# Performance work log

Measured on AMD Instinct MI355X. Metric: run time of the kernel, lower is better.

The kernel has to match this reference:

```python
import jax, jax.numpy as jnp
import numpy as np

LOG2 = float(np.log(2.0))

def ssp(v):
    # shifted softplus: log(0.5*e^v + 0.5)
    return jax.nn.softplus(v) - jnp.asarray(LOG2, v.dtype)

def lora_dense(h, W, b, A, B):
    # base GEMM + per-sample (modulated) low-rank correction; scale = alpha/rank = 1
    base = jnp.einsum('b...i,io->b...o', h, W) + b
    lora = jnp.einsum('b...r,bro->b...o', jnp.einsum('b...i,bir->b...r', h, A), B)
    return ssp(base + lora)

def setup_inputs() -> dict:
    key = jax.random.key(0)
    ks = jax.random.split(key, 32)
    Bsz, Atoms, F, Rbf, R = 2, 512, 128, 64, 4
    d = {}
    d['x'] = jax.random.normal(ks[0], (Bsz, Atoms, F), jnp.float32)
    d['f_ij'] = jax.random.uniform(ks[1], (Bsz, Atoms, Atoms, Rbf), jnp.float32)
    d['c_ij'] = jax.random.uniform(ks[2], (Bsz, Atoms, Atoms), jnp.float32)
    d['mask'] = jax.random.randint(ks[3], (Bsz, Atoms, Atoms), 0, 2, jnp.int32)
    def mk(i, din, dout):
        return (jax.random.normal(ks[4+4*i], (din, dout), jnp.float32) * (1.0/np.sqrt(din)),
                jnp.zeros((dout,), jnp.float32),
                jax.random.normal(ks[5+4*i], (Bsz, din, R), jnp.float32) * 0.05,
                jax.random.normal(ks[6+4*i], (Bsz, R, dout), jnp.float32) * 0.05)
    d['W_bc'], d['b_bc'], d['A_bc'], d['B_bc'] = mk(0, F, F)      # atomwise_bc: F -> dim_filter(=F)
    d['W_f0'], d['b_f0'], d['A_f0'], d['B_f0'] = mk(1, Rbf, F)    # dis_filter layer0
    d['W_f1'], d['b_f1'], d['A_f1'], d['B_f1'] = mk(2, F, F)      # dis_filter layer1
    d['W_f2'], d['b_f2'], d['A_f2'], d['B_f2'] = mk(3, F, F)      # dis_filter layer2
    d['W_a0'], d['b_a0'], d['A_a0'], d['B_a0'] = mk(4, F, F)      # atomwise_ac layer0
    d['W_a1'], d['b_a1'], d['A_a1'], d['B_a1'] = mk(5, F, F)      # atomwise_ac layer1
    return d

def reference(x, f_ij, c_ij, mask,
              W_bc, b_bc, A_bc, B_bc,
              W_f0, b_f0, A_f0, B_f0,
              W_f1, b_f1, A_f1, B_f1,
              W_f2, b_f2, A_f2, B_f2,
              W_a0, b_a0, A_a0, B_a0,
              W_a1, b_a1, A_a1, B_a1):
    x_i = lora_dense(x, W_bc, b_bc, A_bc, B_bc)                 # (B, A, Fdim)
    h = lora_dense(f_ij, W_f0, b_f0, A_f0, B_f0)                # (B, A, A, Fdim)
    h = lora_dense(h, W_f1, b_f1, A_f1, B_f1)
    h = lora_dense(h, W_f2, b_f2, A_f2, B_f2)
    w_ij = h * c_ij[..., None]                                  # (B, A, A, Fdim)
    # x_ij = expand_dims(x_i, -3): neighbor-j features broadcast over receiver i
    y = x_i[:, None, :, :] * w_ij                               # (B, A, A, Fdim)
    y = y * mask[..., None].astype(y.dtype)
    y = jnp.sum(y, axis=-2)                                     # masked neighbor sum -> (B, A, Fdim)
    y = lora_dense(y, W_a0, b_a0, A_a0, B_a0)
    y = lora_dense(y, W_a1, b_a1, A_a1, B_a1)
    return x + y
```

## Files before the change

### kernel.cpp

```cpp
#include <hip/hip_runtime.h>
#include <hip/hip_bf16.h>


typedef float        f32x4  __attribute__((ext_vector_type(4)));
typedef unsigned int u32x4  __attribute__((ext_vector_type(4)));
typedef unsigned int u32x2  __attribute__((ext_vector_type(2)));
typedef __bf16       bf16x8 __attribute__((ext_vector_type(8)));

__device__ __forceinline__ float ssp_pre(float acc, float bpre) {
  float t = __builtin_amdgcn_exp2f(__builtin_fmaf(acc, 1.44269504089f, bpre));
  return 0.69314718056f * __builtin_amdgcn_logf(__builtin_fmaf(t, 0.5f, 0.5f));
}

__device__ __forceinline__ float ssp_f(float v) {
  float t = __builtin_amdgcn_exp2f(v * 1.44269504089f);
  return 0.69314718056f * __builtin_amdgcn_logf(__builtin_fmaf(t, 0.5f, 0.5f));
}

__device__ __forceinline__ unsigned short f2bfu(float f) {
  __hip_bfloat16 h = __float2bfloat16(f);
  return __builtin_bit_cast(unsigned short, h);
}

__device__ __forceinline__ u32x4 pack8(f32x4 a, f32x4 b) {
  u32x4 u;
  u.x = (unsigned)f2bfu(a.x) | ((unsigned)f2bfu(a.y) << 16);
  u.y = (unsigned)f2bfu(a.z) | ((unsigned)f2bfu(a.w) << 16);
  u.z = (unsigned)f2bfu(b.x) | ((unsigned)f2bfu(b.y) << 16);
  u.w = (unsigned)f2bfu(b.z) | ((unsigned)f2bfu(b.w) << 16);
  return u;
}

__device__ __forceinline__ f32x4 fzero4() { f32x4 z = {0.f, 0.f, 0.f, 0.f}; return z; }

#define SWZ(j) (((j) & 7) << 4)

__global__ void prep_weights(
    const float* __restrict__ W_bc, const float* __restrict__ A_bc, const float* __restrict__ B_bc,
    const float* __restrict__ W_f0, const float* __restrict__ A_f0, const float* __restrict__ B_f0,
    const float* __restrict__ W_f1, const float* __restrict__ A_f1, const float* __restrict__ B_f1,
    const float* __restrict__ W_f2, const float* __restrict__ A_f2, const float* __restrict__ B_f2,
    const float* __restrict__ W_a0, const float* __restrict__ A_a0, const float* __restrict__ B_a0,
    const float* __restrict__ W_a1, const float* __restrict__ A_a1, const float* __restrict__ B_a1,
    unsigned short* __restrict__ Wt0, unsigned short* __restrict__ Wt1, unsigned short* __restrict__ Wt2,
    float* __restrict__ Wbc, float* __restrict__ Wa0, float* __restrict__ Wa1)
{
  const int l = blockIdx.y, b = blockIdx.z;
  const int e = blockIdx.x * 256 + threadIdx.x;
  const float *W, *A, *Bm; int din;
  switch (l) {
    case 0:  W = W_bc; A = A_bc; Bm = B_bc; din = 128; break;
    case 1:  W = W_f0; A = A_f0; Bm = B_f0; din = 64;  break;
    case 2:  W = W_f1; A = A_f1; Bm = B_f1; din = 128; break;
    case 3:  W = W_f2; A = A_f2; Bm = B_f2; din = 128; break;
    case 4:  W = W_a0; A = A_a0; Bm = B_a0; din = 128; break;
    default: W = W_a1; A = A_a1; Bm = B_a1; din = 128; break;
  }
  if (e >= din * 128) return;
  const int k = e >> 7, n = e & 127;
  float wv = W[k * 128 + n];
  #pragma unroll
  for (int r = 0; r < 4; ++r)
    wv += A[(b * din + k) * 4 + r] * Bm[(b * 4 + r) * 128 + n];
  if (l == 1)      Wt0[(b * 128 + n) * 64  + k] = f2bfu(wv);
  else if (l == 2) Wt1[(b * 128 + n) * 128 + k] = f2bfu(wv);
  else if (l == 3) Wt2[(b * 128 + n) * 128 + k] = f2bfu(wv);
  else if (l == 0) Wbc[(b * 128 + k) * 128 + n] = wv;
  else if (l == 4) Wa0[(b * 128 + k) * 128 + n] = wv;
  else             Wa1[(b * 128 + k) * 128 + n] = wv;
}

__global__ __launch_bounds__(512) void dense_ssp(
    const float* __restrict__ in, const float* __restrict__ in2,
    const float* __restrict__ W, const float* __restrict__ bias,
    const float* __restrict__ resid, float* __restrict__ out)
{
  __shared__ float in_l[4][128];
  const int t = threadIdx.x;
  const int rg0 = blockIdx.x << 2;
  const int b = rg0 >> 9;
  {
    float v = in[rg0 * 128 + t];
    if (in2) v += in2[rg0 * 128 + t];
    in_l[t >> 7][t & 127] = v;
  }
  __syncthreads();
  const int j = t >> 7, n = t & 127;
  const float* wp = W + (b << 14) + n;
  const float* ip = in_l[j];
  float acc = 0.f;
  #pragma unroll 8
  for (int k = 0; k < 128; ++k) acc += ip[k] * wp[k << 7];
  float r = ssp_f(acc + bias[n]);
  const int oi = (rg0 + j) * 128 + n;
  if (resid) r += resid[oi];
  out[oi] = r;
}

__global__ __launch_bounds__(256, 4) void schnet_core(
    const float* __restrict__ f_ij, const float* __restrict__ c_ij,
    const int* __restrict__ mask,
    const unsigned short* __restrict__ Wt0, const unsigned short* __restrict__ Wt1,
    const unsigned short* __restrict__ Wt2,
    const float* __restrict__ bias0, const float* __restrict__ bias1,
    const float* __restrict__ bias2,
    const float* __restrict__ xi, float* __restrict__ ypart)
{
  __shared__ __align__(16) unsigned short fbuf[64 * 64];
  __shared__ __align__(16) unsigned short hbuf[64 * 128];
  __shared__ int   jlist[576];
  __shared__ float slist[576];
  __shared__ float bias_l[384];
  __shared__ int cnt_s[8], base_s[8], nact_s;

  const int tid  = threadIdx.x;
  const int lane = tid & 63;
  const int w    = tid >> 6;
  const int lrow = lane & 15;
  const int lgrp = lane >> 4;
  const int g    = blockIdx.x;
  const int bi   = g >> 1;
  const int h    = g & 1;
  const int b    = bi >> 9;

  for (int t = tid; t < 384; t += 256) {
    const float* bp = (t < 128) ? bias0 : (t < 256) ? bias1 : bias2;
    bias_l[t] = bp[t & 127] * 1.44269504089f;
  }

  const int mb = bi << 9;
  const int jA = tid, jB = tid + 256;
  const int   mA = mask[mb + jA]; const float cA = c_ij[mb + jA];
  const int   mB = mask[mb + jB]; const float cB = c_ij[mb + jB];
  unsigned long long balA = __ballot(mA != 0);
  unsigned long long balB = __ballot(mB != 0);
  if (lane == 0) { cnt_s[w] = __popcll(balA); cnt_s[4 + w] = __popcll(balB); }
  __syncthreads();
  if (tid == 0) {
    int s = 0;
    for (int c = 0; c < 8; ++c) { base_s[c] = s; s += cnt_s[c]; }
    nact_s = s;
  }
  __syncthreads();
  const int na = nact_s;
  const unsigned long long lm = (1ull << lane) - 1ull;
  if (mA) { int p = base_s[w]     + __popcll(balA & lm); jlist[p] = jA; slist[p] = cA; }
  if (mB) { int p = base_s[4 + w] + __popcll(balB & lm); jlist[p] = jB; slist[p] = cB; }
  if (tid < 64) { int idx = na + tid; if (idx < 576) { jlist[idx] = 0; slist[idx] = 0.f; } }
  __syncthreads();

  const int tiles = (na + 63) >> 6;
  const int tmid  = (tiles + 1) >> 1;
  const int t0 = h ? tmid : 0;
  const int t1 = h ? tiles : tmid;

  const int mg = w;
  float accy[2][4] = {{0.f,0.f,0.f,0.f},{0.f,0.f,0.f,0.f}};
  const float* fbase = f_ij + ((size_t)mb << 6);

  const int wbase0 = ((b << 7) + mg * 32 + lrow) * 64  + (lgrp << 3);
  const int wbase1 = ((b << 7) + mg * 32 + lrow) * 128 + (lgrp << 3);

  for (int tt = t0; tt < t1; ++tt) {
    const int jt0 = tt << 6;
    {
      const int r = tid >> 2, part = tid & 3;
      const int ja = jlist[jt0 + r];
      const f32x4* src = (const f32x4*)(fbase + ja * 64 + part * 16);
      f32x4 v0 = src[0], v1 = src[1], v2 = src[2], v3 = src[3];
      char* dst = (char*)fbuf + r * 128;
      const int o0 = (part * 32) ^ SWZ(r);
      *(u32x4*)(dst + o0)        = pack8(v0, v1);
      *(u32x4*)(dst + (o0 ^ 16)) = pack8(v2, v3);
    }
    __syncthreads();

    f32x4 acc[2][4];

    {
      const unsigned short* wp = Wt0 + wbase0;
      asm volatile("" : "+v"(wp));
      bf16x8 wf[2][2];
      #pragma unroll
      for (int nt = 0; nt < 2; ++nt)
        #pragma unroll
        for (int ks = 0; ks < 2; ++ks)
          wf[nt][ks] = *(const bf16x8*)(wp + nt * (16 * 64) + ks * 32);
      #pragma unroll
      for (int nt = 0; nt < 2; ++nt)
        #pragma unroll
        for (int jt = 0; jt < 4; ++jt) acc[nt][jt] = fzero4();
      #pragma unroll
      for (int jt = 0; jt < 4; ++jt) {
        const int j = jt * 16 + lrow;
        const char* rb = (const char*)fbuf + j * 128;
        const int sw = SWZ(j);
        #pragma unroll
        for (int ks = 0; ks < 2; ++ks) {
          bf16x8 bf = *(const bf16x8*)(rb + ((lgrp * 16 + ks * 64) ^ sw));
          acc[0][jt] = __builtin_amdgcn_mfma_f32_16x16x32_bf16(wf[0][ks], bf, acc[0][jt], 0, 0, 0);
          acc[1][jt] = __builtin_amdgcn_mfma_f32_16x16x32_bf16(wf[1][ks], bf, acc[1][jt], 0, 0, 0);
        }
      }
    }
    {
      f32x4 bp0 = *(const f32x4*)(bias_l +       mg * 32 + 0  + lgrp * 4);
      f32x4 bp1 = *(const f32x4*)(bias_l +       mg * 32 + 16 + lgrp * 4);
      #pragma unroll
      for (int jt = 0; jt < 4; ++jt) {
        const int j = jt * 16 + lrow;
        char* rb = (char*)hbuf + j * 256;
        const int sw = SWZ(j);
        #pragma unroll
        for (int nt = 0; nt < 2; ++nt) {
          const int n0 = mg * 32 + nt * 16 + lgrp * 4;
          const f32x4 bp = nt ? bp1 : bp0;
          float e0 = ssp_pre(acc[nt][jt].x, bp.x);
          float e1 = ssp_pre(acc[nt][jt].y, bp.y);
          float e2 = ssp_pre(acc[nt][jt].z, bp.z);
          float e3 = ssp_pre(acc[nt][jt].w, bp.w);
          u32x2 pk;
          pk.x = (unsigned)f2bfu(e0) | ((unsigned)f2bfu(e1) << 16);
          pk.y = (unsigned)f2bfu(e2) | ((unsigned)f2bfu(e3) << 16);
          *(u32x2*)(rb + ((n0 * 2) ^ sw)) = pk;
        }
      }
    }
    __syncthreads();

    {
      const unsigned short* wp = Wt1 + wbase1;
      asm volatile("" : "+v"(wp));
      bf16x8 wf[2][4];
      #pragma unroll
      for (int nt = 0; nt < 2; ++nt)
        #pragma unroll
        for (int ks = 0; ks < 4; ++ks)
          wf[nt][ks] = *(const bf16x8*)(wp + nt * (16 * 128) + ks * 32);
      #pragma unroll
      for (int nt = 0; nt < 2; ++nt)
        #pragma unroll
        for (int jt = 0; jt < 4; ++jt) acc[nt][jt] = fzero4();
      #pragma unroll
      for (int jt = 0; jt < 4; ++jt) {
        const int j = jt * 16 + lrow;
        const char* rb = (const char*)hbuf + j * 256;
        const int sw = SWZ(j);
        #pragma unroll
        for (int ks = 0; ks < 4; ++ks) {
          bf16x8 bf = *(const bf16x8*)(rb + ((lgrp * 16 + ks * 64) ^ sw));
          acc[0][jt] = __builtin_amdgcn_mfma_f32_16x16x32_bf16(wf[0][ks], bf, acc[0][jt], 0, 0, 0);
          acc[1][jt] = __builtin_amdgcn_mfma_f32_16x16x32_bf16(wf[1][ks], bf, acc[1][jt], 0, 0, 0);
        }
      }
    }
    __syncthreads();
    {
      f32x4 bp0 = *(const f32x4*)(bias_l + 128 + mg * 32 + 0  + lgrp * 4);
      f32x4 bp1 = *(const f32x4*)(bias_l + 128 + mg * 32 + 16 + lgrp * 4);
      #pragma unroll
      for (int jt = 0; jt < 4; ++jt) {
        const int j = jt * 16 + lrow;
        char* rb = (char*)hbuf + j * 256;
        const int sw = SWZ(j);
        #pragma unroll
        for (int nt = 0; nt < 2; ++nt) {
          const int n0 = mg * 32 + nt * 16 + lgrp * 4;
          const f32x4 bp = nt ? bp1 : bp0;
          float e0 = ssp_pre(acc[nt][jt].x, bp.x);
          float e1 = ssp_pre(acc[nt][jt].y, bp.y);
          float e2 = ssp_pre(acc[nt][jt].z, bp.z);
          float e3 = ssp_pre(acc[nt][jt].w, bp.w);
          u32x2 pk;
          pk.x = (unsigned)f2bfu(e0) | ((unsigned)f2bfu(e1) << 16);
          pk.y = (unsigned)f2bfu(e2) | ((unsigned)f2bfu(e3) << 16);
          *(u32x2*)(rb + ((n0 * 2) ^ sw)) = pk;
        }
      }
    }
    __syncthreads();

    {
      const unsigned short* wp = Wt2 + wbase1;
      asm volatile("" : "+v"(wp));
      bf16x8 wf[2][4];
      #pragma unroll
      for (int nt = 0; nt < 2; ++nt)
        #pragma unroll
        for (int ks = 0; ks < 4; ++ks)
          wf[nt][ks] = *(const bf16x8*)(wp + nt * (16 * 128) + ks * 32);
      #pragma unroll
      for (int nt = 0; nt < 2; ++nt)
        #pragma unroll
        for (int jt = 0; jt < 4; ++jt) acc[nt][jt] = fzero4();
      #pragma unroll
      for (int jt = 0; jt < 4; ++jt) {
        const int j = jt * 16 + lrow;
        const char* rb = (const char*)hbuf + j * 256;
        const int sw = SWZ(j);
        #pragma unroll
        for (int ks = 0; ks < 4; ++ks) {
          bf16x8 bf = *(const bf16x8*)(rb + ((lgrp * 16 + ks * 64) ^ sw));
          acc[0][jt] = __builtin_amdgcn_mfma_f32_16x16x32_bf16(wf[0][ks], bf, acc[0][jt], 0, 0, 0);
          acc[1][jt] = __builtin_amdgcn_mfma_f32_16x16x32_bf16(wf[1][ks], bf, acc[1][jt], 0, 0, 0);
        }
      }
    }
    {
      f32x4 bp0 = *(const f32x4*)(bias_l + 256 + mg * 32 + 0  + lgrp * 4);
      f32x4 bp1 = *(const f32x4*)(bias_l + 256 + mg * 32 + 16 + lgrp * 4);
      #pragma unroll
      for (int jt = 0; jt < 4; ++jt) {
        const int jj = jt * 16 + lrow;
        const float s  = slist[jt0 + jj];
        const int   ja = jlist[jt0 + jj];
        const float* xr = xi + (((b << 9) + ja) << 7);
        #pragma unroll
        for (int nt = 0; nt < 2; ++nt) {
          const int n0 = mg * 32 + nt * 16 + lgrp * 4;
          const f32x4 bp = nt ? bp1 : bp0;
          f32x4 xv = *(const f32x4*)(xr + n0);
          float h0 = ssp_pre(acc[nt][jt].x, bp.x);
          float h1 = ssp_pre(acc[nt][jt].y, bp.y);
          float h2 = ssp_pre(acc[nt][jt].z, bp.z);
          float h3 = ssp_pre(acc[nt][jt].w, bp.w);
          accy[nt][0] += s * xv.x * h0;
          accy[nt][1] += s * xv.y * h1;
          accy[nt][2] += s * xv.z * h2;
          accy[nt][3] += s * xv.w * h3;
        }
      }
    }
    __syncthreads();
  }

  #pragma unroll
  for (int d = 1; d < 16; d <<= 1)
    #pragma unroll
    for (int nt = 0; nt < 2; ++nt)
      #pragma unroll
      for (int r = 0; r < 4; ++r)
        accy[nt][r] += __shfl_xor(accy[nt][r], d, 64);
  if (lrow == 0) {
    float* yo = ypart + ((size_t)h << 17) + ((size_t)bi << 7);
    #pragma unroll
    for (int nt = 0; nt < 2; ++nt) {
      const int n0 = mg * 32 + nt * 16 + lgrp * 4;
      f32x4 v = {accy[nt][0], accy[nt][1], accy[nt][2], accy[nt][3]};
      *(f32x4*)(yo + n0) = v;
    }
  }
}

extern "C" void kernel_launch(void* const* d_in, const int* in_sizes, int n_in,
                              void* d_out, int out_size, void* d_ws, size_t ws_size,
                              hipStream_t stream)
{
  const float* x    = (const float*)d_in[0];
  const float* f_ij = (const float*)d_in[1];
  const float* c_ij = (const float*)d_in[2];
  const int*   mask = (const int*)d_in[3];
  const float* W_bc = (const float*)d_in[4];
  const float* b_bc = (const float*)d_in[5];
  const float* A_bc = (const float*)d_in[6];
  const float* B_bc = (const float*)d_in[7];
  const float* W_f0 = (const float*)d_in[8];
  const float* b_f0 = (const float*)d_in[9];
  const float* A_f0 = (const float*)d_in[10];
  const float* B_f0 = (const float*)d_in[11];
  const float* W_f1 = (const float*)d_in[12];
  const float* b_f1 = (const float*)d_in[13];
  const float* A_f1 = (const float*)d_in[14];
  const float* B_f1 = (const float*)d_in[15];
  const float* W_f2 = (const float*)d_in[16];
  const float* b_f2 = (const float*)d_in[17];
  const float* A_f2 = (const float*)d_in[18];
  const float* B_f2 = (const float*)d_in[19];
  const float* W_a0 = (const float*)d_in[20];
  const float* b_a0 = (const float*)d_in[21];
  const float* A_a0 = (const float*)d_in[22];
  const float* B_a0 = (const float*)d_in[23];
  const float* W_a1 = (const float*)d_in[24];
  const float* b_a1 = (const float*)d_in[25];
  const float* A_a1 = (const float*)d_in[26];
  const float* B_a1 = (const float*)d_in[27];
  float* out = (float*)d_out;

  char* ws = (char*)d_ws;
  unsigned short* Wt0 = (unsigned short*)(ws);
  unsigned short* Wt1 = (unsigned short*)(ws + 32768);
  unsigned short* Wt2 = (unsigned short*)(ws + 98304);
  float* Wbc = (float*)(ws + 163840);
  float* Wa0 = (float*)(ws + 294912);
  float* Wa1 = (float*)(ws + 425984);
  float* xi  = (float*)(ws + 557056);
  float* yp  = (float*)(ws + 1081344);
  float* y1  = (float*)(ws + 2129920);

  prep_weights<<<dim3(64, 6, 2), 256, 0, stream>>>(
      W_bc, A_bc, B_bc, W_f0, A_f0, B_f0, W_f1, A_f1, B_f1,
      W_f2, A_f2, B_f2, W_a0, A_a0, B_a0, W_a1, A_a1, B_a1,
      Wt0, Wt1, Wt2, Wbc, Wa0, Wa1);

  dense_ssp<<<256, 512, 0, stream>>>(x, nullptr, Wbc, b_bc, nullptr, xi);

  schnet_core<<<2048, 256, 0, stream>>>(f_ij, c_ij, mask, Wt0, Wt1, Wt2,
                                        b_f0, b_f1, b_f2, xi, yp);

  dense_ssp<<<256, 512, 0, stream>>>(yp, yp + (1 << 17), Wa0, b_a0, nullptr, y1);
  dense_ssp<<<256, 512, 0, stream>>>(y1, nullptr, Wa1, b_a1, x, out);
}
```

Measured before the change: 113.3 us.

## Hoist filter weights to registers, prefetch f_ij tiles, double-buffer h, fuse output denses

The core kernel now loads all three filter-layer weight fragments into registers once per block instead of once per tile. It also prefetches the next tile's f_ij rows into registers while the current tile computes. Alternating two LDS h-buffers removes two barriers per tile, and the last two atomwise dense layers are fused into one kernel, saving a launch and an intermediate round-trip. The extra registers and LDS reduce occupancy, so launch bounds drop from 4 to 3 waves per SIMD, which may limit latency hiding.

Result: slower. 120.0 us (+6.0%).

```diff
diff --git a/kernel.cpp b/kernel.cpp
--- a/kernel.cpp
+++ b/kernel.cpp
@@ -71,19 +71,14 @@
 }
 
 __global__ __launch_bounds__(512) void dense_ssp(
-    const float* __restrict__ in, const float* __restrict__ in2,
-    const float* __restrict__ W, const float* __restrict__ bias,
-    const float* __restrict__ resid, float* __restrict__ out)
+    const float* __restrict__ in, const float* __restrict__ W,
+    const float* __restrict__ bias, float* __restrict__ out)
 {
   __shared__ float in_l[4][128];
   const int t = threadIdx.x;
   const int rg0 = blockIdx.x << 2;
   const int b = rg0 >> 9;
-  {
-    float v = in[rg0 * 128 + t];
-    if (in2) v += in2[rg0 * 128 + t];
-    in_l[t >> 7][t & 127] = v;
-  }
+  in_l[t >> 7][t & 127] = in[rg0 * 128 + t];
   __syncthreads();
   const int j = t >> 7, n = t & 127;
   const float* wp = W + (b << 14) + n;
@@ -91,13 +86,44 @@
   float acc = 0.f;
   #pragma unroll 8
   for (int k = 0; k < 128; ++k) acc += ip[k] * wp[k << 7];
-  float r = ssp_f(acc + bias[n]);
-  const int oi = (rg0 + j) * 128 + n;
-  if (resid) r += resid[oi];
-  out[oi] = r;
-}
-
-__global__ __launch_bounds__(256, 4) void schnet_core(
+  out[(rg0 + j) * 128 + n] = ssp_f(acc + bias[n]);
+}
+
+__global__ __launch_bounds__(512) void dense2_ssp(
+    const float* __restrict__ in, const float* __restrict__ in2,
+    const float* __restrict__ W0, const float* __restrict__ b0,
+    const float* __restrict__ W1, const float* __restrict__ b1,
+    const float* __restrict__ resid, float* __restrict__ out)
+{
+  __shared__ float in_l[4][128];
+  __shared__ float h_l[4][128];
+  const int t = threadIdx.x;
+  const int rg0 = blockIdx.x << 2;
+  const int b = rg0 >> 9;
+  in_l[t >> 7][t & 127] = in[rg0 * 128 + t] + in2[rg0 * 128 + t];
+  __syncthreads();
+  const int j = t >> 7, n = t & 127;
+  {
+    const float* wp = W0 + (b << 14) + n;
+    const float* ip = in_l[j];
+    float acc = 0.f;
+    #pragma unroll 8
+    for (int k = 0; k < 128; ++k) acc += ip[k] * wp[k << 7];
+    h_l[j][n] = ssp_f(acc + b0[n]);
+  }
+  __syncthreads();
+  {
+    const float* wp = W1 + (b << 14) + n;
+    const float* ip = h_l[j];
+    float acc = 0.f;
+    #pragma unroll 8
+    for (int k = 0; k < 128; ++k) acc += ip[k] * wp[k << 7];
+    const int oi = (rg0 + j) * 128 + n;
+    out[oi] = ssp_f(acc + b1[n]) + resid[oi];
+  }
+}
+
+__global__ __launch_bounds__(256, 3) void schnet_core(
     const float* __restrict__ f_ij, const float* __restrict__ c_ij,
     const int* __restrict__ mask,
     const unsigned short* __restrict__ Wt0, const unsigned short* __restrict__ Wt1,
@@ -107,7 +133,8 @@
     const float* __restrict__ xi, float* __restrict__ ypart)
 {
   __shared__ __align__(16) unsigned short fbuf[64 * 64];
-  __shared__ __align__(16) unsigned short hbuf[64 * 128];
+  __shared__ __align__(16) unsigned short hA[64 * 128];
+  __shared__ __align__(16) unsigned short hB[64 * 128];
   __shared__ int   jlist[576];
   __shared__ float slist[576];
   __shared__ float bias_l[384];
@@ -155,61 +182,78 @@
   const int t1 = h ? tiles : tmid;
 
   const int mg = w;
+  const float* fbase = f_ij + ((size_t)mb << 6);
+
+  bf16x8 w0f[2][2], w1f[2][4], w2f[2][4];
+  #pragma unroll
+  for (int nt = 0; nt < 2; ++nt) {
+    const int nout = mg * 32 + nt * 16 + lrow;
+    const int nb0 = (b * 128 + nout) * 64  + lgrp * 8;
+    const int nb1 = (b * 128 + nout) * 128 + lgrp * 8;
+    #pragma unroll
+    for (int ks = 0; ks < 2; ++ks)
+      w0f[nt][ks] = *(const bf16x8*)(Wt0 + nb0 + ks * 32);
+    #pragma unroll
+    for (int ks = 0; ks < 4; ++ks) {
+      w1f[nt][ks] = *(const bf16x8*)(Wt1 + nb1 + ks * 32);
+      w2f[nt][ks] = *(const bf16x8*)(Wt2 + nb1 + ks * 32);
+    }
+  }
+
   float accy[2][4] = {{0.f,0.f,0.f,0.f},{0.f,0.f,0.f,0.f}};
-  const float* fbase = f_ij + ((size_t)mb << 6);
-
-  const int wbase0 = ((b << 7) + mg * 32 + lrow) * 64  + (lgrp << 3);
-  const int wbase1 = ((b << 7) + mg * 32 + lrow) * 128 + (lgrp << 3);
+
+  const int r    = tid >> 2;
+  const int part = tid & 3;
+  f32x4 pre0, pre1, pre2, pre3;
+  {
+    const int pf = (t0 < t1) ? (t0 << 6) : 0;
+    const int ja = jlist[pf + r];
+    const f32x4* src = (const f32x4*)(fbase + ja * 64 + part * 16);
+    pre0 = src[0]; pre1 = src[1]; pre2 = src[2]; pre3 = src[3];
+  }
 
   for (int tt = t0; tt < t1; ++tt) {
     const int jt0 = tt << 6;
     {
-      const int r = tid >> 2, part = tid & 3;
-      const int ja = jlist[jt0 + r];
-      const f32x4* src = (const f32x4*)(fbase + ja * 64 + part * 16);
-      f32x4 v0 = src[0], v1 = src[1], v2 = src[2], v3 = src[3];
       char* dst = (char*)fbuf + r * 128;
       const int o0 = (part * 32) ^ SWZ(r);
-      *(u32x4*)(dst + o0)        = pack8(v0, v1);
-      *(u32x4*)(dst + (o0 ^ 16)) = pack8(v2, v3);
+      *(u32x4*)(dst + o0)        = pack8(pre0, pre1);
+      *(u32x4*)(dst + (o0 ^ 16)) = pack8(pre2, pre3);
     }
     __syncthreads();
 
+    {
+      const int nx = (tt + 1 < t1) ? ((tt + 1) << 6) : jt0;
+      const int ja = jlist[nx + r];
+      const f32x4* src = (const f32x4*)(fbase + ja * 64 + part * 16);
+      pre0 = src[0]; pre1 = src[1]; pre2 = src[2]; pre3 = src[3];
+    }
+
     f32x4 acc[2][4];
 
+    #pragma unroll
+    for (int nt = 0; nt < 2; ++nt)
+      #pragma unroll
+      for (int jt = 0; jt < 4; ++jt) acc[nt][jt] = fzero4();
+    #pragma unroll
+    for (int jt = 0; jt < 4; ++jt) {
+      const int j = jt * 16 + lrow;
+      const char* rb = (const char*)fbuf + j * 128;
+      const int sw = SWZ(j);
+      #pragma unroll
+      for (int ks = 0; ks < 2; ++ks) {
+        bf16x8 bf = *(const bf16x8*)(rb + ((lgrp * 16 + ks * 64) ^ sw));
+        acc[0][jt] = __builtin_amdgcn_mfma_f32_16x16x32_bf16(w0f[0][ks], bf, acc[0][jt], 0, 0, 0);
+        acc[1][jt] = __builtin_amdgcn_mfma_f32_16x16x32_bf16(w0f[1][ks], bf, acc[1][jt], 0, 0, 0);
+      }
+    }
     {
-      const unsigned short* wp = Wt0 + wbase0;
-      asm volatile("" : "+v"(wp));
-      bf16x8 wf[2][2];
-      #pragma unroll
-      for (int nt = 0; nt < 2; ++nt)
-        #pragma unroll
-        for (int ks = 0; ks < 2; ++ks)
-          wf[nt][ks] = *(const bf16x8*)(wp + nt * (16 * 64) + ks * 32);
-      #pragma unroll
-      for (int nt = 0; nt < 2; ++nt)
-        #pragma unroll
-        for (int jt = 0; jt < 4; ++jt) acc[nt][jt] = fzero4();
+      f32x4 bp0 = *(const f32x4*)(bias_l + mg * 32 + 0  + lgrp * 4);
+      f32x4 bp1 = *(const f32x4*)(bias_l + mg * 32 + 16 + lgrp * 4);
       #pragma unroll
       for (int jt = 0; jt < 4; ++jt) {
         const int j = jt * 16 + lrow;
-        const char* rb = (const char*)fbuf + j * 128;
-        const int sw = SWZ(j);
-        #pragma unroll
-        for (int ks = 0; ks < 2; ++ks) {
-          bf16x8 bf = *(const bf16x8*)(rb + ((lgrp * 16 + ks * 64) ^ sw));
-          acc[0][jt] = __builtin_amdgcn_mfma_f32_16x16x32_bf16(wf[0][ks], bf, acc[0][jt], 0, 0, 0);
-          acc[1][jt] = __builtin_amdgcn_mfma_f32_16x16x32_bf16(wf[1][ks], bf, acc[1][jt], 0, 0, 0);
-        }
-      }
-    }
-    {
-      f32x4 bp0 = *(const f32x4*)(bias_l +       mg * 32 + 0  + lgrp * 4);
-      f32x4 bp1 = *(const f32x4*)(bias_l +       mg * 32 + 16 + lgrp * 4);
-      #pragma unroll
-      for (int jt = 0; jt < 4; ++jt) {
-        const int j = jt * 16 + lrow;
-        char* rb = (char*)hbuf + j * 256;
+        char* rb = (char*)hA + j * 256;
         const int sw = SWZ(j);
         #pragma unroll
         for (int nt = 0; nt < 2; ++nt) {
@@ -228,40 +272,29 @@
     }
     __syncthreads();
 
-    {
-      const unsigned short* wp = Wt1 + wbase1;
-      asm volatile("" : "+v"(wp));
-      bf16x8 wf[2][4];
-      #pragma unroll
-      for (int nt = 0; nt < 2; ++nt)
-        #pragma unroll
-        for (int ks = 0; ks < 4; ++ks)
-          wf[nt][ks] = *(const bf16x8*)(wp + nt * (16 * 128) + ks * 32);
-      #pragma unroll
-      for (int nt = 0; nt < 2; ++nt)
-        #pragma unroll
-        for (int jt = 0; jt < 4; ++jt) acc[nt][jt] = fzero4();
-      #pragma unroll
-      for (int jt = 0; jt < 4; ++jt) {
-        const int j = jt * 16 + lrow;
-        const char* rb = (const char*)hbuf + j * 256;
-        const int sw = SWZ(j);
-        #pragma unroll
-        for (int ks = 0; ks < 4; ++ks) {
-          bf16x8 bf = *(const bf16x8*)(rb + ((lgrp * 16 + ks * 64) ^ sw));
-          acc[0][jt] = __builtin_amdgcn_mfma_f32_16x16x32_bf16(wf[0][ks], bf, acc[0][jt], 0, 0, 0);
-          acc[1][jt] = __builtin_amdgcn_mfma_f32_16x16x32_bf16(wf[1][ks], bf, acc[1][jt], 0, 0, 0);
-        }
-      }
-    }
-    __syncthreads();
+    #pragma unroll
+    for (int nt = 0; nt < 2; ++nt)
+      #pragma unroll
+      for (int jt = 0; jt < 4; ++jt) acc[nt][jt] = fzero4();
+    #pragma unroll
+    for (int jt = 0; jt < 4; ++jt) {
+      const int j = jt * 16 + lrow;
+      const char* rb = (const char*)hA + j * 256;
+      const int sw = SWZ(j);
+      #pragma unroll
+      for (int ks = 0; ks < 4; ++ks) {
+        bf16x8 bf = *(const bf16x8*)(rb + ((lgrp * 16 + ks * 64) ^ sw));
+        acc[0][jt] = __builtin_amdgcn_mfma_f32_16x16x32_bf16(w1f[0][ks], bf, acc[0][jt], 0, 0, 0);
+        acc[1][jt] = __builtin_amdgcn_mfma_f32_16x16x32_bf16(w1f[1][ks], bf, acc[1][jt], 0, 0, 0);
+      }
+    }
     {
       f32x4 bp0 = *(const f32x4*)(bias_l + 128 + mg * 32 + 0  + lgrp * 4);
       f32x4 bp1 = *(const f32x4*)(bias_l + 128 + mg * 32 + 16 + lgrp * 4);
       #pragma unroll
       for (int jt = 0; jt < 4; ++jt) {
         const int j = jt * 16 + lrow;
-        char* rb = (char*)hbuf + j * 256;
+        char* rb = (char*)hB + j * 256;
         const int sw = SWZ(j);
         #pragma unroll
         for (int nt = 0; nt < 2; ++nt) {
@@ -280,30 +313,20 @@
     }
     __syncthreads();
 
-    {
-      const unsigned short* wp = Wt2 + wbase1;
-      asm volatile("" : "+v"(wp));
-      bf16x8 wf[2][4];
-      #pragma unroll
-      for (int nt = 0; nt < 2; ++nt)
-        #pragma unroll
-        for (int ks = 0; ks < 4; ++ks)
-          wf[nt][ks] = *(const bf16x8*)(wp + nt * (16 * 128) + ks * 32);
-      #pragma unroll
-      for (int nt = 0; nt < 2; ++nt)
-        #pragma unroll
-        for (int jt = 0; jt < 4; ++jt) acc[nt][jt] = fzero4();
-      #pragma unroll
-      for (int jt = 0; jt < 4; ++jt) {
-        const int j = jt * 16 + lrow;
-        const char* rb = (const char*)hbuf + j * 256;
-        const int sw = SWZ(j);
-        #pragma unroll
-        for (int ks = 0; ks < 4; ++ks) {
-          bf16x8 bf = *(const bf16x8*)(rb + ((lgrp * 16 + ks * 64) ^ sw));
-          acc[0][jt] = __builtin_amdgcn_mfma_f32_16x16x32_bf16(wf[0][ks], bf, acc[0][jt], 0, 0, 0);
-          acc[1][jt] = __builtin_amdgcn_mfma_f32_16x16x32_bf16(wf[1][ks], bf, acc[1][jt], 0, 0, 0);
-        }
+    #pragma unroll
+    for (int nt = 0; nt < 2; ++nt)
+      #pragma unroll
+      for (int jt = 0; jt < 4; ++jt) acc[nt][jt] = fzero4();
+    #pragma unroll
+    for (int jt = 0; jt < 4; ++jt) {
+      const int j = jt * 16 + lrow;
+      const char* rb = (const char*)hB + j * 256;
+      const int sw = SWZ(j);
+      #pragma unroll
+      for (int ks = 0; ks < 4; ++ks) {
+        bf16x8 bf = *(const bf16x8*)(rb + ((lgrp * 16 + ks * 64) ^ sw));
+        acc[0][jt] = __builtin_amdgcn_mfma_f32_16x16x32_bf16(w2f[0][ks], bf, acc[0][jt], 0, 0, 0);
+        acc[1][jt] = __builtin_amdgcn_mfma_f32_16x16x32_bf16(w2f[1][ks], bf, acc[1][jt], 0, 0, 0);
       }
     }
     {
@@ -331,7 +354,6 @@
         }
       }
     }
-    __syncthreads();
   }
 
   #pragma unroll
@@ -339,8 +361,8 @@
     #pragma unroll
     for (int nt = 0; nt < 2; ++nt)
       #pragma unroll
-      for (int r = 0; r < 4; ++r)
-        accy[nt][r] += __shfl_xor(accy[nt][r], d, 64);
+      for (int rr = 0; rr < 4; ++rr)
+        accy[nt][rr] += __shfl_xor(accy[nt][rr], d, 64);
   if (lrow == 0) {
     float* yo = ypart + ((size_t)h << 17) + ((size_t)bi << 7);
     #pragma unroll
@@ -395,18 +417,17 @@
   float* Wa1 = (float*)(ws + 425984);
   float* xi  = (float*)(ws + 557056);
   float* yp  = (float*)(ws + 1081344);
-  float* y1  = (float*)(ws + 2129920);
 
   prep_weights<<<dim3(64, 6, 2), 256, 0, stream>>>(
       W_bc, A_bc, B_bc, W_f0, A_f0, B_f0, W_f1, A_f1, B_f1,
       W_f2, A_f2, B_f2, W_a0, A_a0, B_a0, W_a1, A_a1, B_a1,
       Wt0, Wt1, Wt2, Wbc, Wa0, Wa1);
 
-  dense_ssp<<<256, 512, 0, stream>>>(x, nullptr, Wbc, b_bc, nullptr, xi);
+  dense_ssp<<<256, 512, 0, stream>>>(x, Wbc, b_bc, xi);
 
   schnet_core<<<2048, 256, 0, stream>>>(f_ij, c_ij, mask, Wt0, Wt1, Wt2,
                                         b_f0, b_f1, b_f2, xi, yp);
 
-  dense_ssp<<<256, 512, 0, stream>>>(yp, yp + (1 << 17), Wa0, b_a0, nullptr, y1);
-  dense_ssp<<<256, 512, 0, stream>>>(y1, nullptr, Wa1, b_a1, x, out);
-}
+  dense2_ssp<<<256, 512, 0, stream>>>(yp, yp + (1 << 17), Wa0, b_a0,
+                                      Wa1, b_a1, x, out);
+}
```
